# Optimization experiments

Hardware: AMD Instinct MI355X
Metric: run time of the kernel (lower is better)

## Reference

```python
import jax, jax.numpy as jnp
import numpy as np

T, N, D, FF, H, L, WND = 32, 512, 128, 2048, 8, 2, 8
EPS = 1e-5


def setup_inputs() -> dict:
    key = jax.random.key(0)
    kit = iter(jax.random.split(key, 64))

    def w(shape, scale=0.02):
        return jax.random.normal(next(kit), shape, jnp.float32) * scale

    inp = {"x": jax.random.normal(next(kit), (T, N, D), jnp.float32)}
    # plain transformer encoder (1 layer) params
    inp["enc_in_proj_w"] = w((3 * D, D)); inp["enc_in_proj_b"] = jnp.zeros((3 * D,), jnp.float32)
    inp["enc_out_proj_w"] = w((D, D));    inp["enc_out_proj_b"] = jnp.zeros((D,), jnp.float32)
    inp["enc_lin1_w"] = w((FF, D));       inp["enc_lin1_b"] = jnp.zeros((FF,), jnp.float32)
    inp["enc_lin2_w"] = w((D, FF));       inp["enc_lin2_b"] = jnp.zeros((D,), jnp.float32)
    inp["enc_ln1_w"] = jnp.ones((D,), jnp.float32); inp["enc_ln1_b"] = jnp.zeros((D,), jnp.float32)
    inp["enc_ln2_w"] = jnp.ones((D,), jnp.float32); inp["enc_ln2_b"] = jnp.zeros((D,), jnp.float32)
    # qk transformer encoder (L layers, stacked params)
    inp["qk_in_proj_w"] = w((L, 3 * D, D)); inp["qk_in_proj_b"] = jnp.zeros((L, 3 * D), jnp.float32)
    inp["qk_out_proj_w"] = w((L, D, D));    inp["qk_out_proj_b"] = jnp.zeros((L, D), jnp.float32)
    inp["qk_lin1_w"] = w((L, FF, D));       inp["qk_lin1_b"] = jnp.zeros((L, FF), jnp.float32)
    inp["qk_lin2_w"] = w((L, D, FF));       inp["qk_lin2_b"] = jnp.zeros((L, D), jnp.float32)
    inp["qk_ln1_w"] = jnp.ones((L, D), jnp.float32); inp["qk_ln1_b"] = jnp.zeros((L, D), jnp.float32)
    inp["qk_ln2_w"] = jnp.ones((L, D), jnp.float32); inp["qk_ln2_b"] = jnp.zeros((L, D), jnp.float32)
    # time2vec (SineActivation(1, D))
    inp["t2v_w"] = w((1, D - 1), 1.0); inp["t2v_b"] = w((D - 1,), 1.0)
    inp["t2v_w0"] = w((1, 1), 1.0);    inp["t2v_b0"] = w((1,), 1.0)
    # output head (no bias)
    inp["out_w"] = w((1, D))
    return inp


def _layer_norm(x, g, b):
    m = jnp.mean(x, -1, keepdims=True)
    v = jnp.mean((x - m) ** 2, -1, keepdims=True)
    return (x - m) * jax.lax.rsqrt(v + EPS) * g + b


def _mha(q, k, v, Wi, bi, Wo, bo, mask):
    # q,k,v: [S, B, D] seq-first (torch MultiheadAttention layout)
    S, B, d = q.shape
    dh = d // H
    Wq, Wk, Wv = jnp.split(Wi, 3, axis=0)
    bq, bk, bv = jnp.split(bi, 3, axis=0)
    qh = (q @ Wq.T + bq).reshape(S, B, H, dh)
    kh = (k @ Wk.T + bk).reshape(k.shape[0], B, H, dh)
    vh = (v @ Wv.T + bv).reshape(v.shape[0], B, H, dh)
    scores = jnp.einsum('qbhf,kbhf->bhqk', qh, kh) / np.float32(np.sqrt(dh))
    if mask is not None:
        scores = scores + mask  # additive [S,S] mask broadcast over batch/heads
    a = jax.nn.softmax(scores, axis=-1)
    o = jnp.einsum('bhqk,kbhf->qbhf', a, vh).reshape(S, B, d)
    return o @ Wo.T + bo


def _enc_layer(src, new_v, p, mask):
    # post-LN torch TransformerEncoderLayer (dropout off / eval mode)
    s2 = _mha(src, src, new_v, p['iw'], p['ib'], p['ow'], p['ob'], mask)
    src = _layer_norm(src + s2, p['ln1w'], p['ln1b'])
    h = jax.nn.relu(src @ p['l1w'].T + p['l1b'])
    s2 = h @ p['l2w'].T + p['l2b']
    return _layer_norm(src + s2, p['ln2w'], p['ln2b'])


def _banded_mask():
    # triu(-inf, 1) + triu(-inf, WND).T -> allow i-WND < j <= i
    i = jnp.arange(T)[:, None]
    j = jnp.arange(T)[None, :]
    allowed = (j <= i) & (j > i - WND)
    return jnp.where(allowed, 0.0, -jnp.inf).astype(jnp.float32)


def reference(x, enc_in_proj_w, enc_in_proj_b, enc_out_proj_w, enc_out_proj_b,
              enc_lin1_w, enc_lin1_b, enc_lin2_w, enc_lin2_b,
              enc_ln1_w, enc_ln1_b, enc_ln2_w, enc_ln2_b,
              qk_in_proj_w, qk_in_proj_b, qk_out_proj_w, qk_out_proj_b,
              qk_lin1_w, qk_lin1_b, qk_lin2_w, qk_lin2_b,
              qk_ln1_w, qk_ln1_b, qk_ln2_w, qk_ln2_b,
              t2v_w, t2v_b, t2v_w0, t2v_b0, out_w):
    # 1) plain encoder over the PAIR axis (original transposes before it: seq=N, batch=T)
    xs = jnp.transpose(x, (1, 0, 2))  # [N, T, D]
    p_enc = dict(iw=enc_in_proj_w, ib=enc_in_proj_b, ow=enc_out_proj_w, ob=enc_out_proj_b,
                 l1w=enc_lin1_w, l1b=enc_lin1_b, l2w=enc_lin2_w, l2b=enc_lin2_b,
                 ln1w=enc_ln1_w, ln1b=enc_ln1_b, ln2w=enc_ln2_w, ln2b=enc_ln2_b)
    outs_zs = jnp.transpose(_enc_layer(xs, xs, p_enc, None), (1, 0, 2))  # [T, N, D]
    # 2) time2vec positional signal at tau = 1..T
    tau = jnp.arange(1, T + 1, dtype=jnp.float32)[:, None]  # [T,1]
    t2v = jnp.concatenate([jnp.sin(tau @ t2v_w + t2v_b), tau @ t2v_w0 + t2v_b0], axis=-1)
    out = x + t2v[:, None, :]  # [T, N, D]
    # 3) qk encoder stack with banded causal+window mask, values = outs_zs
    mask = _banded_mask()
    for l in range(L):
        p = dict(iw=qk_in_proj_w[l], ib=qk_in_proj_b[l], ow=qk_out_proj_w[l], ob=qk_out_proj_b[l],
                 l1w=qk_lin1_w[l], l1b=qk_lin1_b[l], l2w=qk_lin2_w[l], l2b=qk_lin2_b[l],
                 ln1w=qk_ln1_w[l], ln1b=qk_ln1_b[l], ln2w=qk_ln2_w[l], ln2b=qk_ln2_b[l])
        out = _enc_layer(out, outs_zs, p, mask)
    return (out @ out_w.T)[..., 0]  # [T, N]
```

## Files before the change

kernel.cpp:

```cpp
#include <hip/hip_runtime.h>
#include <hip/hip_bf16.h>
#include <math.h>

#define TT 32
#define NN 512
#define DD 128
#define FF_ 2048
#define HH 8
#define LL 2
#define WND_ 8
#define TOK (TT*NN)
#define DH 16

typedef __hip_bfloat16 bf16;
typedef __attribute__((ext_vector_type(8))) short bf16x8;
typedef __attribute__((ext_vector_type(4))) float f32x4;

#define GLD_LDS16(gp, lp) __builtin_amdgcn_global_load_lds( \
    (const __attribute__((address_space(1))) unsigned int*)(gp), \
    (__attribute__((address_space(3))) unsigned int*)(lp), 16, 0, 0)

#define MFMA16(a, b, c) __builtin_amdgcn_mfma_f32_16x16x32_bf16((a), (b), (c), 0, 0, 0)

__device__ inline short f2bs(float f) {
    __hip_bfloat16 h = __float2bfloat16(f);
    return *reinterpret_cast<short*>(&h);
}

template<int BM, int BN>
__global__ __launch_bounds__(256) void mfma_gemm(
    const bf16* __restrict__ A, int lda,
    const bf16* __restrict__ W,
    const float* __restrict__ bias,
    bf16* __restrict__ C, int ldc,
    int K, int relu)
{
    constexpr int WM = BM / 2, WN = BN / 2;
    constexpr int FM = WM / 16, FN = WN / 16;
    constexpr int LA = (BM * 64) / (256 * 16);
    constexpr int LB = (BN * 64) / (256 * 16);

    __shared__ bf16 As[BM * 32];
    __shared__ bf16 Bs[BN * 32];

    const int tid  = threadIdx.x;
    const int lane = tid & 63;
    const int wave = tid >> 6;
    const int wm = wave >> 1, wn = wave & 1;
    const int bm = blockIdx.y * BM, bn = blockIdx.x * BN;

    f32x4 acc[FM][FN];
    #pragma unroll
    for (int m = 0; m < FM; m++)
        #pragma unroll
        for (int n = 0; n < FN; n++)
            acc[m][n] = (f32x4){0.f, 0.f, 0.f, 0.f};

    for (int k0 = 0; k0 < K; k0 += 32) {
        #pragma unroll
        for (int i = 0; i < LA; i++) {
            const int o = (tid + i * 256) * 16;
            const int row = o >> 6;
            const int ce  = (o & 63) >> 1;
            GLD_LDS16(A + (size_t)(bm + row) * lda + k0 + ce, (char*)As + o);
        }
        #pragma unroll
        for (int i = 0; i < LB; i++) {
            const int o = (tid + i * 256) * 16;
            const int row = o >> 6;
            const int ce  = (o & 63) >> 1;
            GLD_LDS16(W + (size_t)(bn + row) * K + k0 + ce, (char*)Bs + o);
        }
        __syncthreads();

        bf16x8 af[FM], bfr[FN];
        #pragma unroll
        for (int m = 0; m < FM; m++)
            af[m] = *(const bf16x8*)(As + (wm * WM + m * 16 + (lane & 15)) * 32 + (lane >> 4) * 8);
        #pragma unroll
        for (int n = 0; n < FN; n++)
            bfr[n] = *(const bf16x8*)(Bs + (wn * WN + n * 16 + (lane & 15)) * 32 + (lane >> 4) * 8);
        #pragma unroll
        for (int m = 0; m < FM; m++)
            #pragma unroll
            for (int n = 0; n < FN; n++)
                acc[m][n] = MFMA16(af[m], bfr[n], acc[m][n]);
        __syncthreads();
    }

    #pragma unroll
    for (int n = 0; n < FN; n++) {
        const int col = bn + wn * WN + n * 16 + (lane & 15);
        const float bv = bias[col];
        #pragma unroll
        for (int m = 0; m < FM; m++) {
            #pragma unroll
            for (int r = 0; r < 4; r++) {
                const int row = bm + wm * WM + m * 16 + (lane >> 4) * 4 + r;
                float v = acc[m][n][r] + bv;
                if (relu) v = fmaxf(v, 0.f);
                C[(size_t)row * ldc + col] = __float2bfloat16(v);
            }
        }
    }
}

__global__ __launch_bounds__(256) void mfma_gemm_ln(
    const bf16* __restrict__ A, int lda,
    const bf16* __restrict__ W,
    const float* __restrict__ bias,
    const bf16* __restrict__ R,
    const float* __restrict__ lng, const float* __restrict__ lnb,
    bf16* __restrict__ Y,
    int K)
{
    constexpr int BM = 64, WM = 32, WN = 64, FM = 2, FN = 4;

    __shared__ bf16 As[BM * 32];
    __shared__ bf16 Bs[128 * 32];
    __shared__ float rsum[BM][2];
    __shared__ float rsq[BM][2];

    const int tid  = threadIdx.x;
    const int lane = tid & 63;
    const int wave = tid >> 6;
    const int wm = wave >> 1, wn = wave & 1;
    const int bm = blockIdx.x * BM;

    f32x4 acc[FM][FN];
    #pragma unroll
    for (int m = 0; m < FM; m++)
        #pragma unroll
        for (int n = 0; n < FN; n++)
            acc[m][n] = (f32x4){0.f, 0.f, 0.f, 0.f};

    for (int k0 = 0; k0 < K; k0 += 32) {
        {
            const int o = tid * 16;
            const int row = o >> 6;
            const int ce  = (o & 63) >> 1;
            GLD_LDS16(A + (size_t)(bm + row) * lda + k0 + ce, (char*)As + o);
        }
        #pragma unroll
        for (int i = 0; i < 2; i++) {
            const int o = (tid + i * 256) * 16;
            const int row = o >> 6;
            const int ce  = (o & 63) >> 1;
            GLD_LDS16(W + (size_t)row * K + k0 + ce, (char*)Bs + o);
        }
        __syncthreads();

        bf16x8 af[FM], bfr[FN];
        #pragma unroll
        for (int m = 0; m < FM; m++)
            af[m] = *(const bf16x8*)(As + (wm * WM + m * 16 + (lane & 15)) * 32 + (lane >> 4) * 8);
        #pragma unroll
        for (int n = 0; n < FN; n++)
            bfr[n] = *(const bf16x8*)(Bs + (wn * WN + n * 16 + (lane & 15)) * 32 + (lane >> 4) * 8);
        #pragma unroll
        for (int m = 0; m < FM; m++)
            #pragma unroll
            for (int n = 0; n < FN; n++)
                acc[m][n] = MFMA16(af[m], bfr[n], acc[m][n]);
        __syncthreads();
    }

    #pragma unroll
    for (int n = 0; n < FN; n++) {
        const int col = wn * WN + n * 16 + (lane & 15);
        const float bv = bias[col];
        #pragma unroll
        for (int m = 0; m < FM; m++) {
            #pragma unroll
            for (int r = 0; r < 4; r++) {
                const int rl = wm * WM + m * 16 + (lane >> 4) * 4 + r;
                acc[m][n][r] += bv + __bfloat162float(R[(size_t)(bm + rl) * 128 + col]);
            }
        }
    }

    #pragma unroll
    for (int m = 0; m < FM; m++) {
        #pragma unroll
        for (int r = 0; r < 4; r++) {
            float s = 0.f, q = 0.f;
            #pragma unroll
            for (int n = 0; n < FN; n++) { float v = acc[m][n][r]; s += v; q += v * v; }
            #pragma unroll
            for (int off = 1; off < 16; off <<= 1) {
                s += __shfl_xor(s, off);
                q += __shfl_xor(q, off);
            }
            const int rl = wm * WM + m * 16 + (lane >> 4) * 4 + r;
            if ((lane & 15) == 0) { rsum[rl][wn] = s; rsq[rl][wn] = q; }
        }
    }
    __syncthreads();

    #pragma unroll
    for (int m = 0; m < FM; m++) {
        #pragma unroll
        for (int r = 0; r < 4; r++) {
            const int rl = wm * WM + m * 16 + (lane >> 4) * 4 + r;
            const float S = rsum[rl][0] + rsum[rl][1];
            const float Q = rsq[rl][0] + rsq[rl][1];
            const float mean = S * (1.0f / 128.0f);
            const float var  = Q * (1.0f / 128.0f) - mean * mean;
            const float rstd = rsqrtf(var + 1e-5f);
            #pragma unroll
            for (int n = 0; n < FN; n++) {
                const int col = wn * WN + n * 16 + (lane & 15);
                const float y = (acc[m][n][r] - mean) * rstd * lng[col] + lnb[col];
                Y[(size_t)(bm + rl) * 128 + col] = __float2bfloat16(y);
            }
        }
    }
}

template<bool HEAD>
__global__ __launch_bounds__(512) void ffn_fused(
    const bf16* __restrict__ A,
    const bf16* __restrict__ W1, const float* __restrict__ b1,
    const bf16* __restrict__ W2, const float* __restrict__ b2,
    const float* __restrict__ lng, const float* __restrict__ lnb,
    bf16* __restrict__ Y,
    const float* __restrict__ hw, float* __restrict__ hout)
{
    __shared__ char smem[65536];

    const int tid  = threadIdx.x;
    const int lane = tid & 63;
    const int wv   = tid >> 6;
    const int tt   = wv & 3;
    const int hh   = wv >> 2;
    const int l4   = lane & 15;
    const int g    = lane >> 4;
    const int bm   = blockIdx.x * 64;

    bf16x8 tf[4];
    #pragma unroll
    for (int j = 0; j < 4; j++)
        tf[j] = *(const bf16x8*)(A + (size_t)(bm + tt * 16 + l4) * 128 + j * 32 + g * 8);

    const int q    = tid >> 4;
    const int qq   = q & 15;
    const int piq  = (((qq >> 2) << 3) | (qq & 3)) + ((q >> 4) << 2);
    const int w1cb = ((tid & 15) * 16) ^ ((q & 7) << 4);
    const int w2row = tid >> 2;
    const int w2ce  = ((tid & 3) ^ ((w2row >> 1) & 3)) * 8;

    f32x4 Oacc[8];
    #pragma unroll
    for (int ot = 0; ot < 8; ot++) Oacc[ot] = (f32x4){0.f, 0.f, 0.f, 0.f};

    const f32x4 zz = (f32x4){0.f, 0.f, 0.f, 0.f};
    const int xsw = (l4 & 7) << 4;
    const int w2rsw = (l4 >> 1) & 3;

    auto STAGE = [&](int d, int s) {
        #pragma unroll
        for (int hx = 0; hx < 2; hx++) {
            const int c0 = hx * 1024 + s * 32;
            GLD_LDS16((const char*)W1 + (size_t)(c0 + piq) * 256 + w1cb,
                      smem + d * 16384 + hx * 8192 + tid * 16);
            GLD_LDS16(W2 + (size_t)w2row * 2048 + c0 + w2ce,
                      smem + 32768 + d * 16384 + hx * 8192 + tid * 16);
        }
    };

    STAGE(0, 0);
    for (int s = 0; s < 32; s++) {
        __syncthreads();
        if (s < 31) STAGE((s + 1) & 1, s + 1);
        const int d  = s & 1;
        const int c0 = hh * 1024 + s * 32;
        const char* w1b = smem + d * 16384 + hh * 8192;
        const char* w2b = smem + 32768 + d * 16384 + hh * 8192;

        f32x4 sa0 = zz, sa1 = zz;
        #pragma unroll
        for (int j = 0; j < 4; j++) {
            const int xo = (j * 64 + g * 16) ^ xsw;
            bf16x8 w10 = *(const bf16x8*)(w1b + l4 * 256 + xo);
            bf16x8 w11 = *(const bf16x8*)(w1b + (16 + l4) * 256 + xo);
            sa0 = MFMA16(w10, tf[j], sa0);
            sa1 = MFMA16(w11, tf[j], sa1);
        }
        float4 bv0 = *(const float4*)(b1 + c0 + g * 8);
        float4 bv1 = *(const float4*)(b1 + c0 + g * 8 + 4);
        bf16x8 pf;
        pf[0] = f2bs(fmaxf(sa0[0] + bv0.x, 0.f));
        pf[1] = f2bs(fmaxf(sa0[1] + bv0.y, 0.f));
        pf[2] = f2bs(fmaxf(sa0[2] + bv0.z, 0.f));
        pf[3] = f2bs(fmaxf(sa0[3] + bv0.w, 0.f));
        pf[4] = f2bs(fmaxf(sa1[0] + bv1.x, 0.f));
        pf[5] = f2bs(fmaxf(sa1[1] + bv1.y, 0.f));
        pf[6] = f2bs(fmaxf(sa1[2] + bv1.z, 0.f));
        pf[7] = f2bs(fmaxf(sa1[3] + bv1.w, 0.f));

        #pragma unroll
        for (int ot = 0; ot < 8; ot++) {
            bf16x8 w2f = *(const bf16x8*)(w2b + (ot * 16 + l4) * 64 + ((g ^ w2rsw) << 4));
            Oacc[ot] = MFMA16(pf, w2f, Oacc[ot]);
        }
    }

    __syncthreads();
    if (hh == 1) {
        #pragma unroll
        for (int ot = 0; ot < 8; ot++)
            *(f32x4*)(smem + tt * 8192 + ot * 1024 + lane * 16) = Oacc[ot];
    }
    __syncthreads();
    if (hh == 0) {
        #pragma unroll
        for (int ot = 0; ot < 8; ot++) {
            f32x4 o2 = *(const f32x4*)(smem + tt * 8192 + ot * 1024 + lane * 16);
            Oacc[ot][0] += o2[0]; Oacc[ot][1] += o2[1];
            Oacc[ot][2] += o2[2]; Oacc[ot][3] += o2[3];
        }

        float vv[8][4];
        #pragma unroll
        for (int ot = 0; ot < 8; ot++) {
            const int col = ot * 16 + l4;
            const float bv = b2[col];
            #pragma unroll
            for (int r = 0; r < 4; r++) {
                const int trow = bm + tt * 16 + 4 * g + r;
                vv[ot][r] = Oacc[ot][r] + bv
                          + __bfloat162float(A[(size_t)trow * 128 + col]);
            }
        }

        #pragma unroll
        for (int r = 0; r < 4; r++) {
            float sm = 0.f, qs = 0.f;
            #pragma unroll
            for (int ot = 0; ot < 8; ot++) { float v = vv[ot][r]; sm += v; qs += v * v; }
            #pragma unroll
            for (int off = 1; off < 16; off <<= 1) {
                sm += __shfl_xor(sm, off);
                qs += __shfl_xor(qs, off);
            }
            const float mean = sm * (1.0f / 128.0f);
            const float var  = qs * (1.0f / 128.0f) - mean * mean;
            const float rstd = rsqrtf(var + 1e-5f);
            const int trow = bm + tt * 16 + 4 * g + r;
            float hacc = 0.f;
            #pragma unroll
            for (int ot = 0; ot < 8; ot++) {
                const int col = ot * 16 + l4;
                const float y = (vv[ot][r] - mean) * rstd * lng[col] + lnb[col];
                if (HEAD) hacc += y * hw[col];
                else Y[(size_t)trow * 128 + col] = __float2bfloat16(y);
            }
            if (HEAD) {
                #pragma unroll
                for (int off = 1; off < 16; off <<= 1) hacc += __shfl_xor(hacc, off);
                if (l4 == 0) hout[trow] = hacc;
            }
        }
    }
}

struct ConvDesc {
    const float *x, *s1, *s2, *s3, *s4, *s5, *s6, *s7, *s8;
    bf16 *dx, *d1, *d2, *d3, *d4, *d5, *d6, *d7, *d8;
    const float *w, *b, *w0, *b0;
    float* tbl;
};

__device__ inline void cvt4(const float* s, bf16* d, int j) {
    float4 v = ((const float4*)s)[j];
    ushort4 o;
    o.x = (unsigned short)f2bs(v.x); o.y = (unsigned short)f2bs(v.y);
    o.z = (unsigned short)f2bs(v.z); o.w = (unsigned short)f2bs(v.w);
    *(ushort4*)((unsigned short*)d + j * 4) = o;
}

#define CP0 524288
#define CP1 536576
#define CP2 540672
#define CP3 606208
#define CP4 671744
#define CP5 696320
#define CP6 704512
#define CP7 835584
#define CP8 966656
#define CP9 967680

__global__ __launch_bounds__(256) void conv_all_kernel(ConvDesc cd)
{
    int i = blockIdx.x * 256 + threadIdx.x;
    if (i < CP0)      cvt4(cd.x,  cd.dx, i);
    else if (i < CP1) cvt4(cd.s1, cd.d1, i - CP0);
    else if (i < CP2) cvt4(cd.s2, cd.d2, i - CP1);
    else if (i < CP3) cvt4(cd.s3, cd.d3, i - CP2);
    else if (i < CP4) cvt4(cd.s4, cd.d4, i - CP3);
    else if (i < CP5) cvt4(cd.s5, cd.d5, i - CP4);
    else if (i < CP6) cvt4(cd.s6, cd.d6, i - CP5);
    else if (i < CP7) cvt4(cd.s7, cd.d7, i - CP6);
    else if (i < CP8) cvt4(cd.s8, cd.d8, i - CP7);
    else if (i < CP9) {
        int e = (i - CP8) * 4;
        int t = e >> 7;
        float tau = (float)(t + 1);
        float4 o;
        #pragma unroll
        for (int k = 0; k < 4; k++) {
            int d = (e + k) & 127;
            ((float*)&o)[k] = (d < 127) ? sinf(tau * cd.w[d] + cd.b[d])
                                        : (tau * cd.w0[0] + cd.b0[0]);
        }
        *(float4*)(cd.tbl + e) = o;
    }
}

__global__ __launch_bounds__(256) void attn_full_mfma(
    const bf16* __restrict__ Qkv, bf16* __restrict__ C)
{
    __shared__ bf16 Qs[512 * 16];
    __shared__ bf16 Ks[512 * 16];
    __shared__ bf16 Vt[16 * 520];
    __shared__ bf16 Zero[32];

    const int t = blockIdx.x >> 3;
    const int h = blockIdx.x & 7;
    const int tid = threadIdx.x;

    if (tid < 32) ((unsigned short*)Zero)[tid] = 0;

    for (int n = tid; n < 512; n += 256) {
        const unsigned short* row = (const unsigned short*)Qkv + (size_t)(t * 512 + n) * 384 + h * 16;
        uint4 q0 = *(const uint4*)(row);
        uint4 q1 = *(const uint4*)(row + 8);
        uint4 k0 = *(const uint4*)(row + 128);
        uint4 k1 = *(const uint4*)(row + 136);
        uint4 v0 = *(const uint4*)(row + 256);
        uint4 v1 = *(const uint4*)(row + 264);
        *(uint4*)((unsigned short*)Qs + n * 16)     = q0;
        *(uint4*)((unsigned short*)Qs + n * 16 + 8) = q1;
        *(uint4*)((unsigned short*)Ks + n * 16)     = k0;
        *(uint4*)((unsigned short*)Ks + n * 16 + 8) = k1;
        union { uint4 u[2]; unsigned short s[16]; } vb;
        vb.u[0] = v0; vb.u[1] = v1;
        #pragma unroll
        for (int f = 0; f < 16; f++)
            ((unsigned short*)Vt)[f * 520 + n] = vb.s[f];
    }
    __syncthreads();

    const int lane = tid & 63;
    const int wv   = tid >> 6;
    const int l4   = lane & 15;
    const int g    = lane >> 4;
    const int qbase = wv * 128;
    const bf16* zp = Zero + (g & 1) * 8;
    const int p0 = ((l4 >> 2) << 3) | (l4 & 3);

    bf16x8 qf[8];
    #pragma unroll
    for (int qt = 0; qt < 8; qt++) {
        const bf16* ap = (g < 2) ? (Qs + (qbase + qt * 16 + l4) * 16 + g * 8) : zp;
        qf[qt] = *(const bf16x8*)ap;
    }

    f32x4 Oacc[8];
    float lsum[8];
    #pragma unroll
    for (int qt = 0; qt < 8; qt++) { Oacc[qt] = (f32x4){0.f,0.f,0.f,0.f}; lsum[qt] = 0.f; }

    const float cexp = 0.25f * 1.44269504088896f;

    for (int kt = 0; kt < 16; kt++) {
        const bf16* k0p = (g < 2) ? (Ks + (kt * 32 + p0)     * 16 + g * 8) : zp;
        const bf16* k1p = (g < 2) ? (Ks + (kt * 32 + p0 + 4) * 16 + g * 8) : zp;
        bf16x8 kf0 = *(const bf16x8*)k0p;
        bf16x8 kf1 = *(const bf16x8*)k1p;
        bf16x8 vf  = *(const bf16x8*)(Vt + l4 * 520 + kt * 32 + g * 8);

        #pragma unroll
        for (int qt = 0; qt < 8; qt++) {
            f32x4 z = (f32x4){0.f,0.f,0.f,0.f};
            f32x4 s0 = MFMA16(kf0, qf[qt], z);
            f32x4 s1 = MFMA16(kf1, qf[qt], z);
            float e[8];
            #pragma unroll
            for (int r = 0; r < 4; r++) {
                e[r]     = exp2f(s0[r] * cexp);
                e[4 + r] = exp2f(s1[r] * cexp);
            }
            lsum[qt] += ((e[0]+e[1])+(e[2]+e[3])) + ((e[4]+e[5])+(e[6]+e[7]));
            bf16x8 pf;
            #pragma unroll
            for (int i = 0; i < 8; i++) pf[i] = f2bs(e[i]);
            Oacc[qt] = MFMA16(pf, vf, Oacc[qt]);
        }
    }

    #pragma unroll
    for (int qt = 0; qt < 8; qt++) {
        float ls = lsum[qt];
        ls += __shfl_xor(ls, 16);
        ls += __shfl_xor(ls, 32);
        #pragma unroll
        for (int r = 0; r < 4; r++) {
            float lq = __shfl(ls, g * 4 + r);
            float o = Oacc[qt][r] / lq;
            int qrow = t * 512 + qbase + qt * 16 + g * 4 + r;
            C[(size_t)qrow * 128 + h * 16 + l4] = __float2bfloat16(o);
        }
    }
}

__global__ __launch_bounds__(256) void attn_banded_kernel(
    const bf16* __restrict__ Qkv, const bf16* __restrict__ Vb, bf16* __restrict__ C)
{
    __shared__ float Qs[TT][129];
    __shared__ float Ksh[TT][129];
    __shared__ float Vs[TT][129];
    const int n = blockIdx.x;
    const int tid = threadIdx.x;

    for (int e = tid; e < TT * DD; e += 256) {
        int t = e >> 7, d = e & 127;
        const bf16* row = Qkv + (size_t)(t * NN + n) * 384;
        Qs[t][d]  = __bfloat162float(row[d]);
        Ksh[t][d] = __bfloat162float(row[128 + d]);
        Vs[t][d]  = __bfloat162float(Vb[(size_t)(t * NN + n) * DD + d]);
    }
    __syncthreads();

    const int h = tid >> 5, i = tid & 31;
    const int hb = h * DH;

    float s[WND_];
    #pragma unroll
    for (int kk = 0; kk < WND_; kk++) {
        int j = i - (WND_ - 1) + kk;
        int jc = j < 0 ? 0 : j;
        float d = 0.f;
        #pragma unroll
        for (int f = 0; f < DH; f++) d += Qs[i][hb + f] * Ksh[jc][hb + f];
        s[kk] = (j >= 0) ? d * 0.25f : -1e30f;
    }
    float m = s[0];
    #pragma unroll
    for (int kk = 1; kk < WND_; kk++) m = fmaxf(m, s[kk]);
    float l = 0.f, p[WND_];
    #pragma unroll
    for (int kk = 0; kk < WND_; kk++) { p[kk] = __expf(s[kk] - m); l += p[kk]; }
    float inv = 1.f / l;
    float acc[DH] = {};
    #pragma unroll
    for (int kk = 0; kk < WND_; kk++) {
        int j = i - (WND_ - 1) + kk;
        int jc = j < 0 ? 0 : j;
        float pw = p[kk] * inv;
        #pragma unroll
        for (int f = 0; f < DH; f++) acc[f] += pw * Vs[jc][hb + f];
    }
    bf16* cp = C + (size_t)(i * NN + n) * DD + hb;
    #pragma unroll
    for (int f = 0; f < DH; f++) cp[f] = __float2bfloat16(acc[f]);
}

__global__ __launch_bounds__(256) void t2v_add_kernel(
    const float* __restrict__ x, const float* __restrict__ tbl, bf16* __restrict__ Y)
{
    int i = blockIdx.x * 256 + threadIdx.x;
    int e = i * 4;
    float4 xv = ((const float4*)x)[i];
    int ti = ((e >> 16) << 7) | (e & 127);
    float4 tv = *(const float4*)(tbl + ti);
    ushort4 o;
    o.x = (unsigned short)f2bs(xv.x + tv.x);
    o.y = (unsigned short)f2bs(xv.y + tv.y);
    o.z = (unsigned short)f2bs(xv.z + tv.z);
    o.w = (unsigned short)f2bs(xv.w + tv.w);
    *(ushort4*)((unsigned short*)Y + e) = o;
}


extern "C" void kernel_launch(void* const* d_in, const int* in_sizes, int n_in,
                              void* d_out, int out_size, void* d_ws, size_t ws_size,
                              hipStream_t stream) {
    const float* x           = (const float*)d_in[0];
    const float* enc_in_w    = (const float*)d_in[1];
    const float* enc_in_b    = (const float*)d_in[2];
    const float* enc_out_w   = (const float*)d_in[3];
    const float* enc_out_b   = (const float*)d_in[4];
    const float* enc_l1w     = (const float*)d_in[5];
    const float* enc_l1b     = (const float*)d_in[6];
    const float* enc_l2w     = (const float*)d_in[7];
    const float* enc_l2b     = (const float*)d_in[8];
    const float* enc_ln1w    = (const float*)d_in[9];
    const float* enc_ln1b    = (const float*)d_in[10];
    const float* enc_ln2w    = (const float*)d_in[11];
    const float* enc_ln2b    = (const float*)d_in[12];
    const float* qk_in_w     = (const float*)d_in[13];
    const float* qk_in_b     = (const float*)d_in[14];
    const float* qk_out_w    = (const float*)d_in[15];
    const float* qk_out_b    = (const float*)d_in[16];
    const float* qk_l1w      = (const float*)d_in[17];
    const float* qk_l1b      = (const float*)d_in[18];
    const float* qk_l2w      = (const float*)d_in[19];
    const float* qk_l2b      = (const float*)d_in[20];
    const float* qk_ln1w     = (const float*)d_in[21];
    const float* qk_ln1b     = (const float*)d_in[22];
    const float* qk_ln2w     = (const float*)d_in[23];
    const float* qk_ln2b     = (const float*)d_in[24];
    const float* t2v_w       = (const float*)d_in[25];
    const float* t2v_b       = (const float*)d_in[26];
    const float* t2v_w0      = (const float*)d_in[27];
    const float* t2v_b0      = (const float*)d_in[28];
    const float* out_w       = (const float*)d_in[29];
    float* out = (float*)d_out;

    char* ws = (char*)d_ws;
    const size_t TOKD = (size_t)TOK * DD;
    size_t off = 0;
    auto alloc = [&](size_t bytes) { char* p = ws + off; off += (bytes + 255) & ~(size_t)255; return p; };

    bf16*  Qb   = (bf16*)alloc((size_t)TOK * 384 * 2);
    bf16*  Vb   = (bf16*)alloc(TOKD * 2);
    bf16*  xb   = (bf16*)alloc(TOKD * 2);
    bf16*  bufA = (bf16*)alloc(TOKD * 2);
    bf16*  Zb   = (bf16*)alloc(TOKD * 2);
    bf16*  Cb   = (bf16*)alloc(TOKD * 2);
    float* t2vt = (float*)alloc((size_t)TT * DD * 4);
    bf16* enc_in_wb  = (bf16*)alloc(384 * DD * 2);
    bf16* enc_out_wb = (bf16*)alloc(DD * DD * 2);
    bf16* enc_l1wb   = (bf16*)alloc((size_t)FF_ * DD * 2);
    bf16* enc_l2wb   = (bf16*)alloc((size_t)DD * FF_ * 2);
    bf16* qk_in_wb   = (bf16*)alloc((size_t)LL * 384 * DD * 2);
    bf16* qk_out_wb  = (bf16*)alloc((size_t)LL * DD * DD * 2);
    bf16* qk_l1wb    = (bf16*)alloc((size_t)LL * FF_ * DD * 2);
    bf16* qk_l2wb    = (bf16*)alloc((size_t)LL * DD * FF_ * 2);

    ConvDesc cd;
    cd.x  = x;        cd.dx = xb;
    cd.s1 = enc_in_w; cd.d1 = enc_in_wb;
    cd.s2 = enc_out_w;cd.d2 = enc_out_wb;
    cd.s3 = enc_l1w;  cd.d3 = enc_l1wb;
    cd.s4 = enc_l2w;  cd.d4 = enc_l2wb;
    cd.s5 = qk_in_w;  cd.d5 = qk_in_wb;
    cd.s6 = qk_out_w; cd.d6 = qk_out_wb;
    cd.s7 = qk_l1w;   cd.d7 = qk_l1wb;
    cd.s8 = qk_l2w;   cd.d8 = qk_l2wb;
    cd.w = t2v_w; cd.b = t2v_b; cd.w0 = t2v_w0; cd.b0 = t2v_b0; cd.tbl = t2vt;
    conv_all_kernel<<<(CP9 + 255) / 256, 256, 0, stream>>>(cd);

    auto gemm128 = [&](const bf16* A, int lda, const bf16* W, const float* bias,
                       bf16* C, int ldc, int M, int N, int K, int relu) {
        dim3 grid(N / 128, M / 128);
        mfma_gemm<128, 128><<<grid, 256, 0, stream>>>(A, lda, W, bias, C, ldc, K, relu);
    };
    auto gemm64 = [&](const bf16* A, int lda, const bf16* W, const float* bias,
                      bf16* C, int ldc, int M, int N, int K, int relu) {
        dim3 grid(N / 64, M / 64);
        mfma_gemm<64, 64><<<grid, 256, 0, stream>>>(A, lda, W, bias, C, ldc, K, relu);
    };
    auto gemm_ln = [&](const bf16* A, int lda, const bf16* W, const float* bias,
                       const bf16* R, const float* lng, const float* lnb,
                       bf16* Y, int M, int K) {
        mfma_gemm_ln<<<M / 64, 256, 0, stream>>>(A, lda, W, bias, R, lng, lnb, Y, K);
    };

    gemm128(xb, DD, enc_in_wb, enc_in_b, Qb, 384, TOK, 384, DD, 0);
    attn_full_mfma<<<TT * HH, 256, 0, stream>>>(Qb, Cb);
    gemm_ln(Cb, DD, enc_out_wb, enc_out_b, xb, enc_ln1w, enc_ln1b, bufA, TOK, DD);
    ffn_fused<false><<<TOK / 64, 512, 0, stream>>>(
        bufA, enc_l1wb, enc_l1b, enc_l2wb, enc_l2b,
        enc_ln2w, enc_ln2b, Zb, nullptr, nullptr);

    t2v_add_kernel<<<(TOK * DD / 4) / 256, 256, 0, stream>>>(x, t2vt, bufA);

    for (int l = 0; l < LL; l++) {
        const bf16* iw   = qk_in_wb  + (size_t)l * 384 * DD;
        const float* ib  = qk_in_b   + (size_t)l * 384;
        const bf16* owt  = qk_out_wb + (size_t)l * DD * DD;
        const float* ob  = qk_out_b  + (size_t)l * DD;
        const bf16* l1w  = qk_l1wb   + (size_t)l * FF_ * DD;
        const float* l1b = qk_l1b    + (size_t)l * FF_;
        const bf16* l2w  = qk_l2wb   + (size_t)l * DD * FF_;
        const float* l2b = qk_l2b    + (size_t)l * DD;

        gemm128(bufA, DD, iw, ib, Qb, 384, TOK, 256, DD, 0);
        gemm64(Zb, DD, iw + (size_t)256 * DD, ib + 256, Vb, DD, TOK, DD, DD, 0);
        attn_banded_kernel<<<NN, 256, 0, stream>>>(Qb, Vb, Cb);
        gemm_ln(Cb, DD, owt, ob, bufA, qk_ln1w + l * DD, qk_ln1b + l * DD, bufA, TOK, DD);
        if (l == LL - 1) {
            ffn_fused<true><<<TOK / 64, 512, 0, stream>>>(
                bufA, l1w, l1b, l2w, l2b,
                qk_ln2w + l * DD, qk_ln2b + l * DD, nullptr, out_w, out);
        } else {
            ffn_fused<false><<<TOK / 64, 512, 0, stream>>>(
                bufA, l1w, l1b, l2w, l2b,
                qk_ln2w + l * DD, qk_ln2b + l * DD, bufA, nullptr, nullptr);
        }
    }
}
```

Baseline: 226.2 us.

## Repartition fused FFN waves to reuse weight fragments across two token tiles

Changes the warp split in the fused FFN kernel from 4 token tiles by 2 hidden halves to 2 token groups of two tiles each by 4 hidden quarters. Each wave now applies every W1/W2 LDS fragment to two 16-row token tiles, halving LDS reads per MFMA, and the loop runs 16 stages that each stage four hidden chunks instead of 32 stages of two. In exchange, shared memory doubles to 128 KB, accumulator registers double (about 16 f32x4 outputs plus 8 input fragments), and the final cross-wave reduction now sums four partial results instead of two. The higher register and LDS use may lower occupancy, which is likely one block per CU already.

```diff
diff --git a/kernel.cpp b/kernel.cpp
--- a/kernel.cpp
+++ b/kernel.cpp
@@ -226,21 +226,24 @@
     bf16* __restrict__ Y,
     const float* __restrict__ hw, float* __restrict__ hout)
 {
-    __shared__ char smem[65536];
+    __shared__ char smem[131072];
 
     const int tid  = threadIdx.x;
     const int lane = tid & 63;
     const int wv   = tid >> 6;
-    const int tt   = wv & 3;
-    const int hh   = wv >> 2;
+    const int tg   = wv & 1;
+    const int hq   = wv >> 1;
     const int l4   = lane & 15;
     const int g    = lane >> 4;
     const int bm   = blockIdx.x * 64;
 
-    bf16x8 tf[4];
-    #pragma unroll
-    for (int j = 0; j < 4; j++)
-        tf[j] = *(const bf16x8*)(A + (size_t)(bm + tt * 16 + l4) * 128 + j * 32 + g * 8);
+    bf16x8 tf[2][4];
+    #pragma unroll
+    for (int sub = 0; sub < 2; sub++)
+        #pragma unroll
+        for (int j = 0; j < 4; j++)
+            tf[sub][j] = *(const bf16x8*)(A + (size_t)(bm + (tg * 2 + sub) * 16 + l4) * 128
+                                          + j * 32 + g * 8);
 
     const int q    = tid >> 4;
     const int qq   = q & 15;
@@ -249,116 +252,141 @@
     const int w2row = tid >> 2;
     const int w2ce  = ((tid & 3) ^ ((w2row >> 1) & 3)) * 8;
 
-    f32x4 Oacc[8];
-    #pragma unroll
-    for (int ot = 0; ot < 8; ot++) Oacc[ot] = (f32x4){0.f, 0.f, 0.f, 0.f};
+    auto STAGE = [&](int d, int s) {
+        #pragma unroll
+        for (int hx = 0; hx < 4; hx++) {
+            const int c0 = hx * 512 + s * 32;
+            GLD_LDS16((const char*)W1 + (size_t)(c0 + piq) * 256 + w1cb,
+                      smem + d * 32768 + hx * 8192 + tid * 16);
+            GLD_LDS16(W2 + (size_t)w2row * 2048 + c0 + w2ce,
+                      smem + 65536 + d * 32768 + hx * 8192 + tid * 16);
+        }
+    };
+
+    f32x4 Oacc[2][8];
+    #pragma unroll
+    for (int sub = 0; sub < 2; sub++)
+        #pragma unroll
+        for (int ot = 0; ot < 8; ot++)
+            Oacc[sub][ot] = (f32x4){0.f, 0.f, 0.f, 0.f};
 
     const f32x4 zz = (f32x4){0.f, 0.f, 0.f, 0.f};
     const int xsw = (l4 & 7) << 4;
     const int w2rsw = (l4 >> 1) & 3;
 
-    auto STAGE = [&](int d, int s) {
-        #pragma unroll
-        for (int hx = 0; hx < 2; hx++) {
-            const int c0 = hx * 1024 + s * 32;
-            GLD_LDS16((const char*)W1 + (size_t)(c0 + piq) * 256 + w1cb,
-                      smem + d * 16384 + hx * 8192 + tid * 16);
-            GLD_LDS16(W2 + (size_t)w2row * 2048 + c0 + w2ce,
-                      smem + 32768 + d * 16384 + hx * 8192 + tid * 16);
-        }
-    };
-
     STAGE(0, 0);
-    for (int s = 0; s < 32; s++) {
+    for (int s = 0; s < 16; s++) {
         __syncthreads();
-        if (s < 31) STAGE((s + 1) & 1, s + 1);
+        if (s < 15) STAGE((s + 1) & 1, s + 1);
         const int d  = s & 1;
-        const int c0 = hh * 1024 + s * 32;
-        const char* w1b = smem + d * 16384 + hh * 8192;
-        const char* w2b = smem + 32768 + d * 16384 + hh * 8192;
-
-        f32x4 sa0 = zz, sa1 = zz;
+        const int c0 = hq * 512 + s * 32;
+        const char* w1b = smem + d * 32768 + hq * 8192;
+        const char* w2b = smem + 65536 + d * 32768 + hq * 8192;
+
+        f32x4 sa00 = zz, sa01 = zz, sa10 = zz, sa11 = zz;
         #pragma unroll
         for (int j = 0; j < 4; j++) {
             const int xo = (j * 64 + g * 16) ^ xsw;
             bf16x8 w10 = *(const bf16x8*)(w1b + l4 * 256 + xo);
             bf16x8 w11 = *(const bf16x8*)(w1b + (16 + l4) * 256 + xo);
-            sa0 = MFMA16(w10, tf[j], sa0);
-            sa1 = MFMA16(w11, tf[j], sa1);
+            sa00 = MFMA16(w10, tf[0][j], sa00);
+            sa01 = MFMA16(w10, tf[1][j], sa01);
+            sa10 = MFMA16(w11, tf[0][j], sa10);
+            sa11 = MFMA16(w11, tf[1][j], sa11);
         }
         float4 bv0 = *(const float4*)(b1 + c0 + g * 8);
         float4 bv1 = *(const float4*)(b1 + c0 + g * 8 + 4);
-        bf16x8 pf;
-        pf[0] = f2bs(fmaxf(sa0[0] + bv0.x, 0.f));
-        pf[1] = f2bs(fmaxf(sa0[1] + bv0.y, 0.f));
-        pf[2] = f2bs(fmaxf(sa0[2] + bv0.z, 0.f));
-        pf[3] = f2bs(fmaxf(sa0[3] + bv0.w, 0.f));
-        pf[4] = f2bs(fmaxf(sa1[0] + bv1.x, 0.f));
-        pf[5] = f2bs(fmaxf(sa1[1] + bv1.y, 0.f));
-        pf[6] = f2bs(fmaxf(sa1[2] + bv1.z, 0.f));
-        pf[7] = f2bs(fmaxf(sa1[3] + bv1.w, 0.f));
+        bf16x8 pf0, pf1;
+        pf0[0] = f2bs(fmaxf(sa00[0] + bv0.x, 0.f));
+        pf0[1] = f2bs(fmaxf(sa00[1] + bv0.y, 0.f));
+        pf0[2] = f2bs(fmaxf(sa00[2] + bv0.z, 0.f));
+        pf0[3] = f2bs(fmaxf(sa00[3] + bv0.w, 0.f));
+        pf0[4] = f2bs(fmaxf(sa10[0] + bv1.x, 0.f));
+        pf0[5] = f2bs(fmaxf(sa10[1] + bv1.y, 0.f));
+        pf0[6] = f2bs(fmaxf(sa10[2] + bv1.z, 0.f));
+        pf0[7] = f2bs(fmaxf(sa10[3] + bv1.w, 0.f));
+        pf1[0] = f2bs(fmaxf(sa01[0] + bv0.x, 0.f));
+        pf1[1] = f2bs(fmaxf(sa01[1] + bv0.y, 0.f));
+        pf1[2] = f2bs(fmaxf(sa01[2] + bv0.z, 0.f));
+        pf1[3] = f2bs(fmaxf(sa01[3] + bv0.w, 0.f));
+        pf1[4] = f2bs(fmaxf(sa11[0] + bv1.x, 0.f));
+        pf1[5] = f2bs(fmaxf(sa11[1] + bv1.y, 0.f));
+        pf1[6] = f2bs(fmaxf(sa11[2] + bv1.z, 0.f));
+        pf1[7] = f2bs(fmaxf(sa11[3] + bv1.w, 0.f));
 
         #pragma unroll
         for (int ot = 0; ot < 8; ot++) {
             bf16x8 w2f = *(const bf16x8*)(w2b + (ot * 16 + l4) * 64 + ((g ^ w2rsw) << 4));
-            Oacc[ot] = MFMA16(pf, w2f, Oacc[ot]);
+            Oacc[0][ot] = MFMA16(pf0, w2f, Oacc[0][ot]);
+            Oacc[1][ot] = MFMA16(pf1, w2f, Oacc[1][ot]);
         }
     }
 
     __syncthreads();
-    if (hh == 1) {
-        #pragma unroll
-        for (int ot = 0; ot < 8; ot++)
-            *(f32x4*)(smem + tt * 8192 + ot * 1024 + lane * 16) = Oacc[ot];
+    if (hq != 0) {
+        #pragma unroll
+        for (int sub = 0; sub < 2; sub++)
+            #pragma unroll
+            for (int ot = 0; ot < 8; ot++)
+                *(f32x4*)(smem + tg * 49152 + (hq - 1) * 16384 + (sub * 8 + ot) * 1024
+                          + lane * 16) = Oacc[sub][ot];
     }
     __syncthreads();
-    if (hh == 0) {
-        #pragma unroll
-        for (int ot = 0; ot < 8; ot++) {
-            f32x4 o2 = *(const f32x4*)(smem + tt * 8192 + ot * 1024 + lane * 16);
-            Oacc[ot][0] += o2[0]; Oacc[ot][1] += o2[1];
-            Oacc[ot][2] += o2[2]; Oacc[ot][3] += o2[3];
-        }
-
-        float vv[8][4];
-        #pragma unroll
-        for (int ot = 0; ot < 8; ot++) {
-            const int col = ot * 16 + l4;
-            const float bv = b2[col];
-            #pragma unroll
-            for (int r = 0; r < 4; r++) {
-                const int trow = bm + tt * 16 + 4 * g + r;
-                vv[ot][r] = Oacc[ot][r] + bv
-                          + __bfloat162float(A[(size_t)trow * 128 + col]);
-            }
-        }
-
-        #pragma unroll
-        for (int r = 0; r < 4; r++) {
-            float sm = 0.f, qs = 0.f;
-            #pragma unroll
-            for (int ot = 0; ot < 8; ot++) { float v = vv[ot][r]; sm += v; qs += v * v; }
-            #pragma unroll
-            for (int off = 1; off < 16; off <<= 1) {
-                sm += __shfl_xor(sm, off);
-                qs += __shfl_xor(qs, off);
-            }
-            const float mean = sm * (1.0f / 128.0f);
-            const float var  = qs * (1.0f / 128.0f) - mean * mean;
-            const float rstd = rsqrtf(var + 1e-5f);
-            const int trow = bm + tt * 16 + 4 * g + r;
-            float hacc = 0.f;
+    if (hq == 0) {
+        #pragma unroll
+        for (int p = 0; p < 3; p++)
+            #pragma unroll
+            for (int sub = 0; sub < 2; sub++)
+                #pragma unroll
+                for (int ot = 0; ot < 8; ot++) {
+                    f32x4 o2 = *(const f32x4*)(smem + tg * 49152 + p * 16384
+                                               + (sub * 8 + ot) * 1024 + lane * 16);
+                    Oacc[sub][ot][0] += o2[0]; Oacc[sub][ot][1] += o2[1];
+                    Oacc[sub][ot][2] += o2[2]; Oacc[sub][ot][3] += o2[3];
+                }
+
+        #pragma unroll
+        for (int sub = 0; sub < 2; sub++) {
+            float vv[8][4];
             #pragma unroll
             for (int ot = 0; ot < 8; ot++) {
                 const int col = ot * 16 + l4;
-                const float y = (vv[ot][r] - mean) * rstd * lng[col] + lnb[col];
-                if (HEAD) hacc += y * hw[col];
-                else Y[(size_t)trow * 128 + col] = __float2bfloat16(y);
+                const float bv = b2[col];
+                #pragma unroll
+                for (int r = 0; r < 4; r++) {
+                    const int trow = bm + (tg * 2 + sub) * 16 + 4 * g + r;
+                    vv[ot][r] = Oacc[sub][ot][r] + bv
+                              + __bfloat162float(A[(size_t)trow * 128 + col]);
+                }
             }
-            if (HEAD) {
+
+            #pragma unroll
+            for (int r = 0; r < 4; r++) {
+                float sm = 0.f, qs = 0.f;
                 #pragma unroll
-                for (int off = 1; off < 16; off <<= 1) hacc += __shfl_xor(hacc, off);
-                if (l4 == 0) hout[trow] = hacc;
+                for (int ot = 0; ot < 8; ot++) { float v = vv[ot][r]; sm += v; qs += v * v; }
+                #pragma unroll
+                for (int off = 1; off < 16; off <<= 1) {
+                    sm += __shfl_xor(sm, off);
+                    qs += __shfl_xor(qs, off);
+                }
+                const float mean = sm * (1.0f / 128.0f);
+                const float var  = qs * (1.0f / 128.0f) - mean * mean;
+                const float rstd = rsqrtf(var + 1e-5f);
+                const int trow = bm + (tg * 2 + sub) * 16 + 4 * g + r;
+                float hacc = 0.f;
+                #pragma unroll
+                for (int ot = 0; ot < 8; ot++) {
+                    const int col = ot * 16 + l4;
+                    const float y = (vv[ot][r] - mean) * rstd * lng[col] + lnb[col];
+                    if (HEAD) hacc += y * hw[col];
+                    else Y[(size_t)trow * 128 + col] = __float2bfloat16(y);
+                }
+                if (HEAD) {
+                    #pragma unroll
+                    for (int off = 1; off < 16; off <<= 1) hacc += __shfl_xor(hacc, off);
+                    if (l4 == 0) hout[trow] = hacc;
+                }
             }
         }
     }
```

New measurement: 222.9 us. Within noise of the previous version (-1.5%).
